# Optimization experiments

Measured on AMD Instinct MI355X. Metric: run time of the kernel, lower is better.

Reference implementation:

```python
import jax, jax.numpy as jnp
import numpy as np

N, E, H, R = 16384, 262144, 256, 64
INV_SQRT_3 = 1.0 / np.sqrt(3.0)
INV_SQRT_H = 1.0 / np.sqrt(float(H))
INV_SQRT_2 = 1.0 / np.sqrt(2.0)


def ssilu(t):
    # ScaledSiLU: silu(x) / 0.6
    return jax.nn.silu(t) * (1.0 / 0.6)


def layernorm(x, g, b):
    m = jnp.mean(x, axis=-1, keepdims=True)
    v = jnp.var(x, axis=-1, keepdims=True)
    return (x - m) * jax.lax.rsqrt(v + 1e-5) * g + b


def gated_equivariant_block(x, v, Wv1, Wv2, Wu1, bu1, Wu2, bu2, out_ch):
    # x: [N, Cin], v: [N, 3, Cin]
    vec1 = jnp.linalg.norm(v @ Wv1, axis=-2)          # [N, Cin]
    vec2 = v @ Wv2                                     # [N, 3, out_ch]
    h = ssilu(jnp.concatenate([x, vec1], axis=-1) @ Wu1 + bu1) @ Wu2 + bu2
    xn, vn = h[..., :out_ch], h[..., out_ch:]
    return ssilu(xn), vn[:, None, :] * vec2


def setup_inputs() -> dict:
    key = jax.random.key(0)
    ks = iter(jax.random.split(key, 48))

    def w(shape, fan_in):
        return jax.random.normal(next(ks), shape, jnp.float32) / np.sqrt(float(fan_in))

    return {
        "x": jax.random.normal(next(ks), (N, H), jnp.float32),
        "vec": jax.random.normal(next(ks), (N, 3, H), jnp.float32),
        "edge_rbf": jax.random.uniform(next(ks), (E, R), jnp.float32),
        "edge_vector": jax.random.normal(next(ks), (E, 3), jnp.float32),
        # PaiNNMessage params
        "ln_g": jnp.ones((H,), jnp.float32), "ln_b": jnp.zeros((H,), jnp.float32),
        "W_x1": w((H, H), H), "b_x1": jnp.zeros((H,), jnp.float32),
        "W_x2": w((H, 3 * H), H), "b_x2": jnp.zeros((3 * H,), jnp.float32),
        "W_rbf": w((R, 3 * H), R), "b_rbf": jnp.zeros((3 * H,), jnp.float32),
        # PaiNNUpdate params
        "W_vp": w((H, 2 * H), H),
        "W_xv1": w((2 * H, H), 2 * H), "b_xv1": jnp.zeros((H,), jnp.float32),
        "W_xv2": w((H, 3 * H), H), "b_xv2": jnp.zeros((3 * H,), jnp.float32),
        # PaiNNOutput block 1 (H -> H//2)
        "o1_Wv1": w((H, H), H), "o1_Wv2": w((H, H // 2), H),
        "o1_Wu1": w((2 * H, H), 2 * H), "o1_bu1": jnp.zeros((H,), jnp.float32),
        "o1_Wu2": w((H, H), H), "o1_bu2": jnp.zeros((H,), jnp.float32),
        # PaiNNOutput block 2 (H//2 -> 1)
        "o2_Wv1": w((H // 2, H // 2), H // 2), "o2_Wv2": w((H // 2, 1), H // 2),
        "o2_Wu1": w((H, H // 2), H), "o2_bu1": jnp.zeros((H // 2,), jnp.float32),
        "o2_Wu2": w((H // 2, 2), H // 2), "o2_bu2": jnp.zeros((2,), jnp.float32),
        "edge_index": jax.random.randint(next(ks), (2, E), 0, N),
    }


def reference(x, vec, edge_rbf, edge_vector,
              ln_g, ln_b, W_x1, b_x1, W_x2, b_x2, W_rbf, b_rbf,
              W_vp, W_xv1, b_xv1, W_xv2, b_xv2,
              o1_Wv1, o1_Wv2, o1_Wu1, o1_bu1, o1_Wu2, o1_bu2,
              o2_Wv1, o2_Wv2, o2_Wu1, o2_bu1, o2_Wu2, o2_bu2,
              edge_index):
    src, dst = edge_index[0], edge_index[1]

    # ---- PaiNNMessage ----
    xh = ssilu(layernorm(x, ln_g, ln_b) @ W_x1 + b_x1) @ W_x2 + b_x2   # [N, 3H]
    rbfh = edge_rbf @ W_rbf + b_rbf                                     # [E, 3H]
    m = xh[src] * rbfh                                                  # gather + fuse
    m1, m2, m3 = m[:, :H], m[:, H:2 * H], m[:, 2 * H:]
    m2 = m2 * INV_SQRT_3
    vmsg = (vec[src] * m2[:, None, :] + m3[:, None, :] * edge_vector[:, :, None]) * INV_SQRT_H  # [E,3,H]
    dx = jax.ops.segment_sum(m1, dst, num_segments=N)
    dvec = jax.ops.segment_sum(vmsg, dst, num_segments=N)
    x = x + dx
    vec = vec + dvec

    # ---- PaiNNUpdate ----
    vp = vec @ W_vp                                    # [N, 3, 2H]
    vec1, vec2 = vp[..., :H], vp[..., H:]
    vec_dot = jnp.sum(vec1 * vec2, axis=1) * INV_SQRT_H            # [N, H]
    vnorm = jnp.sqrt(jnp.sum(vec2 * vec2, axis=-2) + 1e-8)          # [N, H]
    xvh = ssilu(jnp.concatenate([x, vnorm], axis=-1) @ W_xv1 + b_xv1) @ W_xv2 + b_xv2
    xv1, xv2, xv3 = xvh[:, :H], xvh[:, H:2 * H], xvh[:, 2 * H:]
    x = x + (xv1 + xv2 * vec_dot) * INV_SQRT_2
    vec = vec + xv3[:, None, :] * vec1

    # ---- PaiNNOutput ----
    x, vec = gated_equivariant_block(x, vec, o1_Wv1, o1_Wv2, o1_Wu1, o1_bu1, o1_Wu2, o1_bu2, H // 2)
    x, vec = gated_equivariant_block(x, vec, o2_Wv1, o2_Wv2, o2_Wu1, o2_bu1, o2_Wu2, o2_bu2, 1)
    return jnp.squeeze(vec, axis=-1)   # [N, 3]
```

## Files before the change

kernel.cpp:

```cpp
#include <hip/hip_runtime.h>
#include <math.h>

#define NN 16384
#define EE 262144
#define HH 256

#define INV_SQRT_3f 0.57735026918962576f
#define INV_SQRT_Hf 0.0625f
#define INV_SQRT_2f 0.70710678118654752f
#define SSILU_SCALE 1.6666666666666667f

typedef __attribute__((ext_vector_type(8))) short bf16x8;
typedef __attribute__((ext_vector_type(4))) float f32x4;

__device__ __forceinline__ float ssilu_f(float v) {
    return v * (1.0f / (1.0f + __expf(-v))) * SSILU_SCALE;
}
__device__ __forceinline__ float b2f(short s) {
    unsigned int u = ((unsigned int)(unsigned short)s) << 16;
    return __uint_as_float(u);
}
__device__ __forceinline__ short f2b(float f) {
    unsigned int u = __float_as_uint(f);
    unsigned int r = (u + 0x7fff + ((u >> 16) & 1)) >> 16;
    return (short)r;
}
__device__ __forceinline__ void cvt8(float4 a, float4 b, bf16x8& h, bf16x8& l) {
    float v[8] = {a.x, a.y, a.z, a.w, b.x, b.y, b.z, b.w};
    #pragma unroll
    for (int j = 0; j < 8; j++) {
        short hh = f2b(v[j]);
        h[j] = hh;
        l[j] = f2b(v[j] - b2f(hh));
    }
}
__device__ __forceinline__ void cvt8v(f32x4 a, f32x4 b, bf16x8& h, bf16x8& l) {
    float v[8] = {a.x, a.y, a.z, a.w, b.x, b.y, b.z, b.w};
    #pragma unroll
    for (int j = 0; j < 8; j++) {
        short hh = f2b(v[j]);
        h[j] = hh;
        l[j] = f2b(v[j] - b2f(hh));
    }
}

__global__ void __launch_bounds__(256) ln_kernel(const float* __restrict__ x,
                                                 const float* __restrict__ g,
                                                 const float* __restrict__ b,
                                                 float* __restrict__ o_,
                                                 float* __restrict__ x1) {
    int n = blockIdx.x;
    int t = threadIdx.x;
    float v = x[(long)n * HH + t];
    x1[(long)n * HH + t] = v;
    float s = v, s2 = v * v;
    #pragma unroll
    for (int off = 32; off > 0; off >>= 1) {
        s  += __shfl_down(s, off);
        s2 += __shfl_down(s2, off);
    }
    __shared__ float red[8];
    int wave = t >> 6, lane = t & 63;
    if (lane == 0) { red[wave] = s; red[4 + wave] = s2; }
    __syncthreads();
    __shared__ float mr[2];
    if (t == 0) {
        float ts = red[0] + red[1] + red[2] + red[3];
        float ts2 = red[4] + red[5] + red[6] + red[7];
        float mean = ts * (1.0f / HH);
        float var = ts2 * (1.0f / HH) - mean * mean;
        mr[0] = mean;
        mr[1] = rsqrtf(var + 1e-5f);
    }
    __syncthreads();
    o_[(long)n * HH + t] = (v - mr[0]) * mr[1] * g[t] + b[t];
}

struct WtArgs {
    const float* W[12];
    int K[12];
    int N[12];
    int off[13];
};

__global__ void __launch_bounds__(256) wt_split_all(WtArgs a,
                                                    short* __restrict__ WTh,
                                                    short* __restrict__ WTl) {
    int idx = blockIdx.x * 256 + threadIdx.x;
    int s = 0;
    #pragma unroll
    for (int i = 1; i < 12; i++) s += (idx >= a.off[i]) ? 1 : 0;
    int local = idx - a.off[s];
    int K = a.K[s], N = a.N[s];
    int k = local / N, n = local - k * N;
    float w = a.W[s][local];
    short hh = f2b(w);
    long o = (long)a.off[s] + (long)n * K + k;
    WTh[o] = hh;
    WTl[o] = f2b(w - b2f(hh));
}

__global__ void __launch_bounds__(256) mfma_gemm(const float* __restrict__ A,
                                                 const short* __restrict__ Wh,
                                                 const short* __restrict__ Wl,
                                                 const float* __restrict__ bias,
                                                 void* __restrict__ C1,
                                                 void* __restrict__ C2,
                                                 int M, int K, int N, int act) {
    int tid = threadIdx.x;
    int wave = tid >> 6, lane = tid & 63;
    int quad = lane >> 4, l16 = lane & 15;
    long bm = (long)blockIdx.x * 128 + wave * 32;
    long bn = (long)blockIdx.y * 64;
    long a0 = (bm + l16) * K + quad * 8;
    long a1 = a0 + (long)16 * K;
    long w0 = (bn + l16) * K + quad * 8;

    f32x4 acc[2][4];
    #pragma unroll
    for (int f = 0; f < 2; f++)
        #pragma unroll
        for (int t = 0; t < 4; t++) acc[f][t] = (f32x4){0.f, 0.f, 0.f, 0.f};

    bf16x8 cah[2], cal[2], cbh[4], cbl[4];
    cvt8(*(const float4*)(A + a0), *(const float4*)(A + a0 + 4), cah[0], cal[0]);
    cvt8(*(const float4*)(A + a1), *(const float4*)(A + a1 + 4), cah[1], cal[1]);
    #pragma unroll
    for (int t = 0; t < 4; t++) {
        long wo = w0 + (long)t * 16 * K;
        cbh[t] = *(const bf16x8*)(Wh + wo);
        cbl[t] = *(const bf16x8*)(Wl + wo);
    }

    for (int k0 = 0; k0 < K; k0 += 32) {
        int k1 = k0 + 32;
        float4 n0a, n0b, n1a, n1b;
        bf16x8 nbh[4], nbl[4];
        if (k1 < K) {
            n0a = *(const float4*)(A + a0 + k1);
            n0b = *(const float4*)(A + a0 + k1 + 4);
            n1a = *(const float4*)(A + a1 + k1);
            n1b = *(const float4*)(A + a1 + k1 + 4);
            #pragma unroll
            for (int t = 0; t < 4; t++) {
                long wo = w0 + (long)t * 16 * K + k1;
                nbh[t] = *(const bf16x8*)(Wh + wo);
                nbl[t] = *(const bf16x8*)(Wl + wo);
            }
        }
        #pragma unroll
        for (int t = 0; t < 4; t++) {
            #pragma unroll
            for (int f = 0; f < 2; f++) {
                acc[f][t] = __builtin_amdgcn_mfma_f32_16x16x32_bf16(cah[f], cbh[t], acc[f][t], 0, 0, 0);
                acc[f][t] = __builtin_amdgcn_mfma_f32_16x16x32_bf16(cal[f], cbh[t], acc[f][t], 0, 0, 0);
                acc[f][t] = __builtin_amdgcn_mfma_f32_16x16x32_bf16(cah[f], cbl[t], acc[f][t], 0, 0, 0);
            }
        }
        if (k1 < K) {
            cvt8(n0a, n0b, cah[0], cal[0]);
            cvt8(n1a, n1b, cah[1], cal[1]);
            #pragma unroll
            for (int t = 0; t < 4; t++) { cbh[t] = nbh[t]; cbl[t] = nbl[t]; }
        }
    }

    #pragma unroll
    for (int f = 0; f < 2; f++) {
        long row0 = bm + f * 16 + quad * 4;
        #pragma unroll
        for (int t = 0; t < 4; t++) {
            long col = bn + t * 16 + l16;
            float bv = bias ? bias[col] : 0.f;
            #pragma unroll
            for (int r = 0; r < 4; r++) {
                float v = acc[f][t][r] + bv;
                long row = row0 + r;
                if (act == 4) {
                    if (col < 256) ((float*)C1)[row * 256 + col] = v;
                    else           ((short*)C2)[row * 256 + col - 256] = f2b(v);
                } else if (act == 5) {
                    if (col < 256) ((short*)C1)[row * 256 + col] = f2b(v);
                    else           ((float*)C2)[row * 128 + col - 256] = v;
                } else {
                    long idx = row * N + col;
                    if (act == 3) {
                        short hh = f2b(v);
                        ((short*)C1)[idx] = hh;
                        ((short*)C2)[idx] = f2b(v - b2f(hh));
                    } else if (act == 2) {
                        ((short*)C1)[idx] = f2b(v);
                    } else {
                        if (act == 1) v = ssilu_f(v);
                        ((float*)C1)[idx] = v;
                    }
                }
            }
        }
    }
}

__global__ void __launch_bounds__(256) zero_kernel(int* __restrict__ p, int n) {
    int i = blockIdx.x * 256 + threadIdx.x;
    if (i < n) p[i] = 0;
}

__global__ void __launch_bounds__(256) hist_kernel(const int* __restrict__ eidx,
                                                   int* __restrict__ cnt) {
    int e = blockIdx.x * 256 + threadIdx.x;
    atomicAdd(&cnt[eidx[EE + e]], 1);
}

__global__ void __launch_bounds__(256) scan_kernel(int* __restrict__ cursor,
                                                   int* __restrict__ rowptr) {
    int t = threadIdx.x;
    int base_i = t * 64;
    int tsum = 0;
    for (int i = 0; i < 64; i++) tsum += cursor[base_i + i];
    __shared__ int ls[256];
    ls[t] = tsum;
    __syncthreads();
    for (int off = 1; off < 256; off <<= 1) {
        int v = (t >= off) ? ls[t - off] : 0;
        __syncthreads();
        ls[t] += v;
        __syncthreads();
    }
    int running = ls[t] - tsum;
    for (int i = 0; i < 64; i++) {
        int c = cursor[base_i + i];
        rowptr[base_i + i] = running;
        cursor[base_i + i] = running;
        running += c;
    }
    if (t == 255) rowptr[NN] = running;
}

__global__ void __launch_bounds__(256) scatter_kernel(const int* __restrict__ eidx,
                                                      const float* __restrict__ ev,
                                                      int* __restrict__ cursor,
                                                      int* __restrict__ perm,
                                                      int* __restrict__ dsts,
                                                      int* __restrict__ srcs,
                                                      float* __restrict__ evs) {
    int e = blockIdx.x * 256 + threadIdx.x;
    int s_ = eidx[e];
    int d_ = eidx[EE + e];
    int pos = atomicAdd(&cursor[d_], 1);
    perm[pos] = e;
    dsts[pos] = d_;
    srcs[pos] = s_;
    evs[pos * 3 + 0] = ev[e * 3 + 0];
    evs[pos * 3 + 1] = ev[e * 3 + 1];
    evs[pos * 3 + 2] = ev[e * 3 + 2];
}

__global__ void __launch_bounds__(512) edge_gather_kernel(
        const float* __restrict__ rbf,
        const short* __restrict__ Wrh,
        const short* __restrict__ Wrl,
        const float* __restrict__ b_rbf,
        const float* __restrict__ xh,
        const float* __restrict__ vec,
        const int* __restrict__ perm,
        const int* __restrict__ dsts,
        const int* __restrict__ srcs,
        const float* __restrict__ evs,
        float* __restrict__ x1,
        float* __restrict__ vecacc) {
    int tid = threadIdx.x;
    int wave = tid >> 6, lane = tid & 63;
    int quad = lane >> 4, l16 = lane & 15;
    int bm = blockIdx.x * 128;
    int base = wave * 16;

    __shared__ __align__(16) float mlds[128][66];
    __shared__ int dst_s[128], src_s[128];
    __shared__ float ev_s[128][3];

    if (lane < 16) {
        int i = base + lane;
        dst_s[i] = __builtin_nontemporal_load(dsts + bm + i);
        src_s[i] = __builtin_nontemporal_load(srcs + bm + i);
        ev_s[i][0] = __builtin_nontemporal_load(evs + (long)(bm + i) * 3 + 0);
        ev_s[i][1] = __builtin_nontemporal_load(evs + (long)(bm + i) * 3 + 1);
        ev_s[i][2] = __builtin_nontemporal_load(evs + (long)(bm + i) * 3 + 2);
    }

    int e0 = __builtin_nontemporal_load(perm + bm + base + l16);
    bf16x8 afh[2], afl[2];
    {
        long ebase = (long)e0 * 64 + quad * 8;
        #pragma unroll
        for (int ks = 0; ks < 2; ks++) {
            f32x4 ua = __builtin_nontemporal_load(
                reinterpret_cast<const f32x4*>(rbf + ebase + ks * 32));
            f32x4 ub = __builtin_nontemporal_load(
                reinterpret_cast<const f32x4*>(rbf + ebase + ks * 32 + 4));
            cvt8v(ua, ub, afh[ks], afl[ks]);
        }
    }

    for (int sec = 0; sec < 3; sec++) {
        for (int tile = 0; tile < 4; tile++) {
            int bn = sec * 256 + tile * 64;
            f32x4 acc[4];
            #pragma unroll
            for (int t = 0; t < 4; t++) {
                float bv = b_rbf[bn + t * 16 + l16];
                acc[t] = (f32x4){bv, bv, bv, bv};
                #pragma unroll
                for (int ks = 0; ks < 2; ks++) {
                    long wo = (long)(bn + t * 16 + l16) * 64 + ks * 32 + quad * 8;
                    bf16x8 bh = *(const bf16x8*)(Wrh + wo);
                    bf16x8 bl = *(const bf16x8*)(Wrl + wo);
                    acc[t] = __builtin_amdgcn_mfma_f32_16x16x32_bf16(afh[ks], bh, acc[t], 0, 0, 0);
                    acc[t] = __builtin_amdgcn_mfma_f32_16x16x32_bf16(afl[ks], bh, acc[t], 0, 0, 0);
                    acc[t] = __builtin_amdgcn_mfma_f32_16x16x32_bf16(afh[ks], bl, acc[t], 0, 0, 0);
                }
            }
            #pragma unroll
            for (int t = 0; t < 4; t++)
                #pragma unroll
                for (int r = 0; r < 4; r++)
                    mlds[base + quad * 4 + r][t * 16 + l16] = acc[t][r];

            int colx = tile * 64 + lane;
            if (sec == 0) {
                float pv[16];
                #pragma unroll
                for (int i = 0; i < 16; i++) {
                    long xb = (long)src_s[base + i] * 768;
                    pv[i] = mlds[base + i][lane] * xh[xb + colx];
                }
                float a = 0.f;
                int dprev = dst_s[base];
                #pragma unroll
                for (int i = 0; i < 16; i++) {
                    int d = dst_s[base + i];
                    if (d != dprev) {
                        atomicAdd(&x1[(long)dprev * 256 + colx], a);
                        a = 0.f;
                        dprev = d;
                    }
                    a += pv[i];
                }
                atomicAdd(&x1[(long)dprev * 256 + colx], a);
            } else if (sec == 1) {
                float a0 = 0.f, a1 = 0.f, a2 = 0.f;
                int dprev = dst_s[base];
                #pragma unroll 1
                for (int b = 0; b < 4; b++) {
                    float p0[4], p1[4], p2[4];
                    #pragma unroll
                    for (int j = 0; j < 4; j++) {
                        int i = b * 4 + j;
                        long xb = (long)src_s[base + i] * 768;
                        float m2 = mlds[base + i][lane] * (INV_SQRT_3f * INV_SQRT_Hf) *
                                   xh[xb + 256 + colx];
                        p0[j] = vec[xb + colx] * m2;
                        p1[j] = vec[xb + 256 + colx] * m2;
                        p2[j] = vec[xb + 512 + colx] * m2;
                    }
                    #pragma unroll
                    for (int j = 0; j < 4; j++) {
                        int i = b * 4 + j;
                        int d = dst_s[base + i];
                        if (d != dprev) {
                            long vb = (long)dprev * 768 + colx;
                            atomicAdd(&vecacc[vb], a0);
                            atomicAdd(&vecacc[vb + 256], a1);
                            atomicAdd(&vecacc[vb + 512], a2);
                            a0 = a1 = a2 = 0.f;
                            dprev = d;
                        }
                        a0 += p0[j]; a1 += p1[j]; a2 += p2[j];
                    }
                }
                long vb = (long)dprev * 768 + colx;
                atomicAdd(&vecacc[vb], a0);
                atomicAdd(&vecacc[vb + 256], a1);
                atomicAdd(&vecacc[vb + 512], a2);
            } else {
                float pm[16];
                #pragma unroll
                for (int i = 0; i < 16; i++) {
                    long xb = (long)src_s[base + i] * 768;
                    pm[i] = mlds[base + i][lane] * INV_SQRT_Hf * xh[xb + 512 + colx];
                }
                float a0 = 0.f, a1 = 0.f, a2 = 0.f;
                int dprev = dst_s[base];
                #pragma unroll
                for (int i = 0; i < 16; i++) {
                    int d = dst_s[base + i];
                    if (d != dprev) {
                        long vb = (long)dprev * 768 + colx;
                        atomicAdd(&vecacc[vb], a0);
                        atomicAdd(&vecacc[vb + 256], a1);
                        atomicAdd(&vecacc[vb + 512], a2);
                        a0 = a1 = a2 = 0.f;
                        dprev = d;
                    }
                    a0 += pm[i] * ev_s[base + i][0];
                    a1 += pm[i] * ev_s[base + i][1];
                    a2 += pm[i] * ev_s[base + i][2];
                }
                long vb = (long)dprev * 768 + colx;
                atomicAdd(&vecacc[vb], a0);
                atomicAdd(&vecacc[vb + 256], a1);
                atomicAdd(&vecacc[vb + 512], a2);
            }
        }
    }
}

__global__ void __launch_bounds__(256) vdot_cat_kernel(const float* __restrict__ vec1,
                                                       const short* __restrict__ vec2,
                                                       const float* __restrict__ x1,
                                                       float* __restrict__ vdot,
                                                       float* __restrict__ cat) {
    int idx = blockIdx.x * 256 + threadIdx.x;
    int n = idx >> 8, h = idx & 255;
    float dsum = 0.f, s2 = 0.f;
    #pragma unroll
    for (int d = 0; d < 3; d++) {
        long r = (long)(n * 3 + d) * 256 + h;
        float a = vec1[r];
        float b = b2f(vec2[r]);
        dsum += a * b;
        s2 += b * b;
    }
    vdot[idx] = dsum * INV_SQRT_Hf;
    cat[(long)n * 512 + h] = x1[idx];
    cat[(long)n * 512 + 256 + h] = sqrtf(s2 + 1e-8f);
}

__global__ void __launch_bounds__(256) e4_kernel(float* __restrict__ x1,
                                                 float* __restrict__ vecacc,
                                                 const float* __restrict__ vec1,
                                                 const float* __restrict__ vdot,
                                                 const short* __restrict__ xvh_h,
                                                 const short* __restrict__ xvh_l) {
    int idx = blockIdx.x * 256 + threadIdx.x;
    int n = idx >> 8, h = idx & 255;
    long b0 = (long)n * 768 + h;
    float xv1 = b2f(xvh_h[b0])       + b2f(xvh_l[b0]);
    float xv2 = b2f(xvh_h[b0 + 256]) + b2f(xvh_l[b0 + 256]);
    float xv3 = b2f(xvh_h[b0 + 512]) + b2f(xvh_l[b0 + 512]);
    x1[idx] = x1[idx] + (xv1 + xv2 * vdot[idx]) * INV_SQRT_2f;
    #pragma unroll
    for (int d = 0; d < 3; d++) {
        long r = (long)(n * 3 + d) * 256 + h;
        vecacc[r] = vecacc[r] + xv3 * vec1[r];
    }
}

__global__ void __launch_bounds__(256) normcat_kernel(const float* __restrict__ xin,
                                                      const short* __restrict__ w,
                                                      float* __restrict__ cat,
                                                      int Cx, int C, int shift) {
    int idx = blockIdx.x * 256 + threadIdx.x;
    int cols = 1 << shift;
    int n = idx >> shift, c = idx & (cols - 1);
    float v;
    if (c < Cx) {
        v = xin[(long)n * Cx + c];
    } else {
        int cc = c - Cx;
        float s = 0.f;
        #pragma unroll
        for (int d = 0; d < 3; d++) {
            float a = b2f(w[(long)(n * 3 + d) * C + cc]);
            s += a * a;
        }
        v = sqrtf(s);
    }
    cat[idx] = v;
}

__global__ void __launch_bounds__(256) gate1_kernel(const float* __restrict__ h1,
                                                    const float* __restrict__ w2,
                                                    float* __restrict__ x3,
                                                    float* __restrict__ vecC) {
    int idx = blockIdx.x * 256 + threadIdx.x;
    int n = idx >> 7, c = idx & 127;
    x3[idx] = ssilu_f(h1[(long)n * 256 + c]);
    float vn = h1[(long)n * 256 + 128 + c];
    #pragma unroll
    for (int d = 0; d < 3; d++) {
        long r = (long)(n * 3 + d) * 128 + c;
        vecC[r] = vn * w2[r];
    }
}

__global__ void __launch_bounds__(256) g12_kernel(const float* __restrict__ vecC,
                                                  const float* __restrict__ Wv2,
                                                  float* __restrict__ w4) {
    int row = blockIdx.x * 4 + (threadIdx.x >> 6);
    int lane = threadIdx.x & 63;
    long r0 = (long)row * 128 + lane;
    float s = vecC[r0] * Wv2[lane] + vecC[r0 + 64] * Wv2[64 + lane];
    #pragma unroll
    for (int off = 32; off > 0; off >>= 1) s += __shfl_down(s, off);
    if (lane == 0) w4[row] = s;
}

__global__ void __launch_bounds__(256) final_kernel(const float* __restrict__ t5,
                                                    const float* __restrict__ Wu2,
                                                    const float* __restrict__ bu2,
                                                    const float* __restrict__ w4,
                                                    float* __restrict__ out) {
    int n = blockIdx.x * 4 + (threadIdx.x >> 6);
    int lane = threadIdx.x & 63;
    float s = t5[(long)n * 128 + lane] * Wu2[lane * 2 + 1] +
              t5[(long)n * 128 + 64 + lane] * Wu2[(64 + lane) * 2 + 1];
    #pragma unroll
    for (int off = 32; off > 0; off >>= 1) s += __shfl_down(s, off);
    float val = __shfl(s, 0) + bu2[1];
    if (lane < 3) out[(long)n * 3 + lane] = val * w4[(long)n * 3 + lane];
}

extern "C" void kernel_launch(void* const* d_in, const int* in_sizes, int n_in,
                              void* d_out, int out_size, void* d_ws, size_t ws_size,
                              hipStream_t stream) {
    const float* x          = (const float*)d_in[0];
    const float* vec        = (const float*)d_in[1];
    const float* edge_rbf   = (const float*)d_in[2];
    const float* edge_vector= (const float*)d_in[3];
    const float* ln_g       = (const float*)d_in[4];
    const float* ln_b       = (const float*)d_in[5];
    const float* W_x1       = (const float*)d_in[6];
    const float* b_x1       = (const float*)d_in[7];
    const float* W_x2       = (const float*)d_in[8];
    const float* b_x2       = (const float*)d_in[9];
    const float* W_rbf      = (const float*)d_in[10];
    const float* b_rbf      = (const float*)d_in[11];
    const float* W_vp       = (const float*)d_in[12];
    const float* W_xv1      = (const float*)d_in[13];
    const float* b_xv1      = (const float*)d_in[14];
    const float* W_xv2      = (const float*)d_in[15];
    const float* b_xv2      = (const float*)d_in[16];
    const float* o1_Wv1     = (const float*)d_in[17];
    const float* o1_Wv2     = (const float*)d_in[18];
    const float* o1_Wu1     = (const float*)d_in[19];
    const float* o1_bu1     = (const float*)d_in[20];
    const float* o1_Wu2     = (const float*)d_in[21];
    const float* o1_bu2     = (const float*)d_in[22];
    const float* o2_Wv1     = (const float*)d_in[23];
    const float* o2_Wv2     = (const float*)d_in[24];
    const float* o2_Wu1     = (const float*)d_in[25];
    const float* o2_bu1     = (const float*)d_in[26];
    const float* o2_Wu2     = (const float*)d_in[27];
    const float* o2_bu2     = (const float*)d_in[28];
    const int*   edge_index = (const int*)d_in[29];
    float* out = (float*)d_out;
    float* ws  = (float*)d_ws;

    const size_t S = (size_t)NN * 256;
    const size_t Q = S / 4;
    float* x1      = ws;
    float* vecacc  = ws + 4 * Q;
    short* wtb     = (short*)(ws + 16 * Q);
    const long WLO = 1114112;
    float* xln   = ws + 18 * Q;
    float* t1    = ws + 22 * Q;
    float* xh    = ws + 30 * Q;
    int* rowptr    = (int*)(ws + 48 * Q);
    int* cursor    = rowptr + (NN + 1);
    int* perm      = cursor + NN;
    int* dsts      = perm + EE;
    int* srcs      = dsts + EE;
    float* evs     = (float*)(srcs + EE);
    float* vec1  = ws + 30 * Q;
    short* vec2b = (short*)(ws + 42 * Q);
    float* vdot  = ws + 48 * Q;
    float* cat   = ws + 18 * Q;
    float* t2    = ws + 26 * Q;
    short* xvh_h = (short*)(ws + 18 * Q);
    short* xvh_l = (short*)(ws + 42 * Q);
    short* w1b   = (short*)(ws + 30 * Q);
    float* w2    = ws + 36 * Q;
    float* cat2  = ws + 42 * Q;
    float* t4    = ws + 18 * Q;
    float* h1    = ws + 22 * Q;
    float* x3    = ws + 26 * Q;
    float* vecC  = ws + 28 * Q;
    short* w3b   = (short*)(ws + 34 * Q);
    float* w4    = ws + 37 * Q;
    float* cat3  = ws + 38 * Q;
    float* t5    = ws + 42 * Q;

    short* WT_x1    = wtb;
    short* WT_x2    = wtb + 65536;
    short* WT_vp    = wtb + 262144;
    short* WT_xv1   = wtb + 393216;
    short* WT_xv2   = wtb + 524288;
    short* WT_o1Wv1 = wtb + 720896;
    short* WT_o1Wv2 = wtb + 786432;
    short* WT_o1Wu1 = wtb + 819200;
    short* WT_o1Wu2 = wtb + 950272;
    short* WT_o2Wv1 = wtb + 1015808;
    short* WT_o2Wu1 = wtb + 1032192;
    short* WT_rbf   = wtb + 1064960;

    WtArgs wa;
    const float* wsrc[12] = {W_x1, W_x2, W_vp, W_xv1, W_xv2, o1_Wv1, o1_Wv2,
                             o1_Wu1, o1_Wu2, o2_Wv1, o2_Wu1, W_rbf};
    int wk[12] = {256, 256, 256, 512, 256, 256, 256, 512, 256, 128, 256, 64};
    int wn[12] = {256, 768, 512, 256, 768, 256, 128, 256, 256, 128, 128, 768};
    int off = 0;
    for (int i = 0; i < 12; i++) {
        wa.W[i] = wsrc[i]; wa.K[i] = wk[i]; wa.N[i] = wn[i];
        wa.off[i] = off; off += wk[i] * wn[i];
    }
    wa.off[12] = off;
    wt_split_all<<<off / 256, 256, 0, stream>>>(wa, wtb, wtb + WLO);

    hipMemcpyAsync(vecacc, vec, 3 * S * sizeof(float), hipMemcpyDeviceToDevice, stream);

    ln_kernel<<<NN, 256, 0, stream>>>(x, ln_g, ln_b, xln, x1);
    mfma_gemm<<<dim3(NN / 128, 4), 256, 0, stream>>>(xln, WT_x1, WT_x1 + WLO,
                                                     b_x1, t1, nullptr, NN, 256, 256, 1);
    mfma_gemm<<<dim3(NN / 128, 12), 256, 0, stream>>>(t1, WT_x2, WT_x2 + WLO,
                                                      b_x2, xh, nullptr, NN, 256, 768, 0);

    zero_kernel<<<(NN + 255) / 256, 256, 0, stream>>>(cursor, NN);
    hist_kernel<<<EE / 256, 256, 0, stream>>>(edge_index, cursor);
    scan_kernel<<<1, 256, 0, stream>>>(cursor, rowptr);
    scatter_kernel<<<EE / 256, 256, 0, stream>>>(edge_index, edge_vector, cursor,
                                                 perm, dsts, srcs, evs);
    edge_gather_kernel<<<EE / 128, 512, 0, stream>>>(
        edge_rbf, WT_rbf, WT_rbf + WLO, b_rbf, xh, vec,
        perm, dsts, srcs, evs, x1, vecacc);

    mfma_gemm<<<dim3(3 * NN / 128, 8), 256, 0, stream>>>(vecacc, WT_vp, WT_vp + WLO,
                                                         nullptr, vec1, vec2b,
                                                         3 * NN, 256, 512, 4);
    vdot_cat_kernel<<<NN, 256, 0, stream>>>(vec1, vec2b, x1, vdot, cat);
    mfma_gemm<<<dim3(NN / 128, 4), 256, 0, stream>>>(cat, WT_xv1, WT_xv1 + WLO,
                                                     b_xv1, t2, nullptr, NN, 512, 256, 1);
    mfma_gemm<<<dim3(NN / 128, 12), 256, 0, stream>>>(t2, WT_xv2, WT_xv2 + WLO,
                                                      b_xv2, xvh_h, xvh_l, NN, 256, 768, 3);
    e4_kernel<<<NN, 256, 0, stream>>>(x1, vecacc, vec1, vdot, xvh_h, xvh_l);

    mfma_gemm<<<dim3(3 * NN / 128, 6), 256, 0, stream>>>(vecacc, WT_o1Wv1, WT_o1Wv1 + WLO,
                                                         nullptr, w1b, w2,
                                                         3 * NN, 256, 384, 5);
    normcat_kernel<<<NN * 512 / 256, 256, 0, stream>>>(x1, w1b, cat2, 256, 256, 9);
    mfma_gemm<<<dim3(NN / 128, 4), 256, 0, stream>>>(cat2, WT_o1Wu1, WT_o1Wu1 + WLO,
                                                     o1_bu1, t4, nullptr, NN, 512, 256, 1);
    mfma_gemm<<<dim3(NN / 128, 4), 256, 0, stream>>>(t4, WT_o1Wu2, WT_o1Wu2 + WLO,
                                                     o1_bu2, h1, nullptr, NN, 256, 256, 0);
    gate1_kernel<<<NN * 128 / 256, 256, 0, stream>>>(h1, w2, x3, vecC);

    mfma_gemm<<<dim3(3 * NN / 128, 2), 256, 0, stream>>>(vecC, WT_o2Wv1, WT_o2Wv1 + WLO,
                                                         nullptr, w3b, nullptr,
                                                         3 * NN, 128, 128, 2);
    g12_kernel<<<3 * NN / 4, 256, 0, stream>>>(vecC, o2_Wv2, w4);
    normcat_kernel<<<NN * 256 / 256, 256, 0, stream>>>(x3, w3b, cat3, 128, 128, 8);
    mfma_gemm<<<dim3(NN / 128, 2), 256, 0, stream>>>(cat3, WT_o2Wu1, WT_o2Wu1 + WLO,
                                                     o2_bu1, t5, nullptr, NN, 256, 128, 1);
    final_kernel<<<NN / 4, 256, 0, stream>>>(t5, o2_Wu2, o2_bu2, w4, out);
}
```

Before: 1.440 ms.

## Merge vec message sections into one atomic pass and fold vec copy into layernorm

The edge kernel used to handle the m2 (vec gather) and m3 (edge-vector) sections in separate passes, each issuing its own atomicAdds into vecacc. Now both MFMA tiles are computed back to back and their contributions are summed before a single set of atomics, which halves the vec-accumulator atomic traffic and the segmented-reduction work. Separately, the device-to-device memcpy that seeds vecacc with vec is folded into ln_kernel, saving one copy launch. The merged loop keeps the pm2/pm3 arrays live in registers at the same time, which raises register pressure in a 512-thread kernel.

Measured after the change: 1.477 ms. +2.5%, slower.

```diff
diff --git a/kernel.cpp b/kernel.cpp
--- a/kernel.cpp
+++ b/kernel.cpp
@@ -45,14 +45,20 @@
 }
 
 __global__ void __launch_bounds__(256) ln_kernel(const float* __restrict__ x,
+                                                 const float* __restrict__ vec,
                                                  const float* __restrict__ g,
                                                  const float* __restrict__ b,
                                                  float* __restrict__ o_,
-                                                 float* __restrict__ x1) {
+                                                 float* __restrict__ x1,
+                                                 float* __restrict__ vecacc) {
     int n = blockIdx.x;
     int t = threadIdx.x;
     float v = x[(long)n * HH + t];
     x1[(long)n * HH + t] = v;
+    long vb = (long)n * 768 + t;
+    vecacc[vb]       = vec[vb];
+    vecacc[vb + 256] = vec[vb + 256];
+    vecacc[vb + 512] = vec[vb + 512];
     float s = v, s2 = v * v;
     #pragma unroll
     for (int off = 32; off > 0; off >>= 1) {
@@ -255,6 +261,35 @@
     evs[pos * 3 + 2] = ev[e * 3 + 2];
 }
 
+__device__ __forceinline__ void mfma_tile(int bn, int base, int quad, int l16,
+                                          const bf16x8 (&afh)[2],
+                                          const bf16x8 (&afl)[2],
+                                          const short* __restrict__ Wrh,
+                                          const short* __restrict__ Wrl,
+                                          const float* __restrict__ b_rbf,
+                                          float (*mlds)[66]) {
+    f32x4 acc[4];
+    #pragma unroll
+    for (int t = 0; t < 4; t++) {
+        float bv = b_rbf[bn + t * 16 + l16];
+        acc[t] = (f32x4){bv, bv, bv, bv};
+        #pragma unroll
+        for (int ks = 0; ks < 2; ks++) {
+            long wo = (long)(bn + t * 16 + l16) * 64 + ks * 32 + quad * 8;
+            bf16x8 bh = *(const bf16x8*)(Wrh + wo);
+            bf16x8 bl = *(const bf16x8*)(Wrl + wo);
+            acc[t] = __builtin_amdgcn_mfma_f32_16x16x32_bf16(afh[ks], bh, acc[t], 0, 0, 0);
+            acc[t] = __builtin_amdgcn_mfma_f32_16x16x32_bf16(afl[ks], bh, acc[t], 0, 0, 0);
+            acc[t] = __builtin_amdgcn_mfma_f32_16x16x32_bf16(afh[ks], bl, acc[t], 0, 0, 0);
+        }
+    }
+    #pragma unroll
+    for (int t = 0; t < 4; t++)
+        #pragma unroll
+        for (int r = 0; r < 4; r++)
+            mlds[base + quad * 4 + r][t * 16 + l16] = acc[t][r];
+}
+
 __global__ void __launch_bounds__(512) edge_gather_kernel(
         const float* __restrict__ rbf,
         const short* __restrict__ Wrh,
@@ -301,116 +336,79 @@
         }
     }
 
-    for (int sec = 0; sec < 3; sec++) {
-        for (int tile = 0; tile < 4; tile++) {
-            int bn = sec * 256 + tile * 64;
-            f32x4 acc[4];
+    for (int tile = 0; tile < 4; tile++) {
+        mfma_tile(tile * 64, base, quad, l16, afh, afl, Wrh, Wrl, b_rbf, mlds);
+        int colx = tile * 64 + lane;
+        float pv[16];
+        #pragma unroll
+        for (int i = 0; i < 16; i++) {
+            long xb = (long)src_s[base + i] * 768;
+            pv[i] = mlds[base + i][lane] * xh[xb + colx];
+        }
+        float a = 0.f;
+        int dprev = dst_s[base];
+        #pragma unroll
+        for (int i = 0; i < 16; i++) {
+            int d = dst_s[base + i];
+            if (d != dprev) {
+                atomicAdd(&x1[(long)dprev * 256 + colx], a);
+                a = 0.f;
+                dprev = d;
+            }
+            a += pv[i];
+        }
+        atomicAdd(&x1[(long)dprev * 256 + colx], a);
+    }
+
+    for (int tile = 0; tile < 4; tile++) {
+        int colx = tile * 64 + lane;
+        mfma_tile(256 + tile * 64, base, quad, l16, afh, afl, Wrh, Wrl, b_rbf, mlds);
+        float pm2[16];
+        #pragma unroll
+        for (int i = 0; i < 16; i++) {
+            long xb = (long)src_s[base + i] * 768;
+            pm2[i] = mlds[base + i][lane] * (INV_SQRT_3f * INV_SQRT_Hf) *
+                     xh[xb + 256 + colx];
+        }
+        mfma_tile(512 + tile * 64, base, quad, l16, afh, afl, Wrh, Wrl, b_rbf, mlds);
+        float pm3[16];
+        #pragma unroll
+        for (int i = 0; i < 16; i++) {
+            long xb = (long)src_s[base + i] * 768;
+            pm3[i] = mlds[base + i][lane] * INV_SQRT_Hf * xh[xb + 512 + colx];
+        }
+        float a0 = 0.f, a1 = 0.f, a2 = 0.f;
+        int dprev = dst_s[base];
+        #pragma unroll 1
+        for (int b = 0; b < 4; b++) {
+            float p0[4], p1[4], p2[4];
             #pragma unroll
-            for (int t = 0; t < 4; t++) {
-                float bv = b_rbf[bn + t * 16 + l16];
-                acc[t] = (f32x4){bv, bv, bv, bv};
-                #pragma unroll
-                for (int ks = 0; ks < 2; ks++) {
-                    long wo = (long)(bn + t * 16 + l16) * 64 + ks * 32 + quad * 8;
-                    bf16x8 bh = *(const bf16x8*)(Wrh + wo);
-                    bf16x8 bl = *(const bf16x8*)(Wrl + wo);
-                    acc[t] = __builtin_amdgcn_mfma_f32_16x16x32_bf16(afh[ks], bh, acc[t], 0, 0, 0);
-                    acc[t] = __builtin_amdgcn_mfma_f32_16x16x32_bf16(afl[ks], bh, acc[t], 0, 0, 0);
-                    acc[t] = __builtin_amdgcn_mfma_f32_16x16x32_bf16(afh[ks], bl, acc[t], 0, 0, 0);
-                }
+            for (int j = 0; j < 4; j++) {
+                int i = b * 4 + j;
+                long xb = (long)src_s[base + i] * 768;
+                p0[j] = vec[xb + colx] * pm2[i]       + ev_s[base + i][0] * pm3[i];
+                p1[j] = vec[xb + 256 + colx] * pm2[i] + ev_s[base + i][1] * pm3[i];
+                p2[j] = vec[xb + 512 + colx] * pm2[i] + ev_s[base + i][2] * pm3[i];
             }
             #pragma unroll
-            for (int t = 0; t < 4; t++)
-                #pragma unroll
-                for (int r = 0; r < 4; r++)
-                    mlds[base + quad * 4 + r][t * 16 + l16] = acc[t][r];
-
-            int colx = tile * 64 + lane;
-            if (sec == 0) {
-                float pv[16];
-                #pragma unroll
-                for (int i = 0; i < 16; i++) {
-                    long xb = (long)src_s[base + i] * 768;
-                    pv[i] = mlds[base + i][lane] * xh[xb + colx];
+            for (int j = 0; j < 4; j++) {
+                int i = b * 4 + j;
+                int d = dst_s[base + i];
+                if (d != dprev) {
+                    long vb = (long)dprev * 768 + colx;
+                    atomicAdd(&vecacc[vb], a0);
+                    atomicAdd(&vecacc[vb + 256], a1);
+                    atomicAdd(&vecacc[vb + 512], a2);
+                    a0 = a1 = a2 = 0.f;
+                    dprev = d;
                 }
-                float a = 0.f;
-                int dprev = dst_s[base];
-                #pragma unroll
-                for (int i = 0; i < 16; i++) {
-                    int d = dst_s[base + i];
-                    if (d != dprev) {
-                        atomicAdd(&x1[(long)dprev * 256 + colx], a);
-                        a = 0.f;
-                        dprev = d;
-                    }
-                    a += pv[i];
-                }
-                atomicAdd(&x1[(long)dprev * 256 + colx], a);
-            } else if (sec == 1) {
-                float a0 = 0.f, a1 = 0.f, a2 = 0.f;
-                int dprev = dst_s[base];
-                #pragma unroll 1
-                for (int b = 0; b < 4; b++) {
-                    float p0[4], p1[4], p2[4];
-                    #pragma unroll
-                    for (int j = 0; j < 4; j++) {
-                        int i = b * 4 + j;
-                        long xb = (long)src_s[base + i] * 768;
-                        float m2 = mlds[base + i][lane] * (INV_SQRT_3f * INV_SQRT_Hf) *
-                                   xh[xb + 256 + colx];
-                        p0[j] = vec[xb + colx] * m2;
-                        p1[j] = vec[xb + 256 + colx] * m2;
-                        p2[j] = vec[xb + 512 + colx] * m2;
-                    }
-                    #pragma unroll
-                    for (int j = 0; j < 4; j++) {
-                        int i = b * 4 + j;
-                        int d = dst_s[base + i];
-                        if (d != dprev) {
-                            long vb = (long)dprev * 768 + colx;
-                            atomicAdd(&vecacc[vb], a0);
-                            atomicAdd(&vecacc[vb + 256], a1);
-                            atomicAdd(&vecacc[vb + 512], a2);
-                            a0 = a1 = a2 = 0.f;
-                            dprev = d;
-                        }
-                        a0 += p0[j]; a1 += p1[j]; a2 += p2[j];
-                    }
-                }
-                long vb = (long)dprev * 768 + colx;
-                atomicAdd(&vecacc[vb], a0);
-                atomicAdd(&vecacc[vb + 256], a1);
-                atomicAdd(&vecacc[vb + 512], a2);
-            } else {
-                float pm[16];
-                #pragma unroll
-                for (int i = 0; i < 16; i++) {
-                    long xb = (long)src_s[base + i] * 768;
-                    pm[i] = mlds[base + i][lane] * INV_SQRT_Hf * xh[xb + 512 + colx];
-                }
-                float a0 = 0.f, a1 = 0.f, a2 = 0.f;
-                int dprev = dst_s[base];
-                #pragma unroll
-                for (int i = 0; i < 16; i++) {
-                    int d = dst_s[base + i];
-                    if (d != dprev) {
-                        long vb = (long)dprev * 768 + colx;
-                        atomicAdd(&vecacc[vb], a0);
-                        atomicAdd(&vecacc[vb + 256], a1);
-                        atomicAdd(&vecacc[vb + 512], a2);
-                        a0 = a1 = a2 = 0.f;
-                        dprev = d;
-                    }
-                    a0 += pm[i] * ev_s[base + i][0];
-                    a1 += pm[i] * ev_s[base + i][1];
-                    a2 += pm[i] * ev_s[base + i][2];
-                }
-                long vb = (long)dprev * 768 + colx;
-                atomicAdd(&vecacc[vb], a0);
-                atomicAdd(&vecacc[vb + 256], a1);
-                atomicAdd(&vecacc[vb + 512], a2);
+                a0 += p0[j]; a1 += p1[j]; a2 += p2[j];
             }
         }
+        long vb = (long)dprev * 768 + colx;
+        atomicAdd(&vecacc[vb], a0);
+        atomicAdd(&vecacc[vb + 256], a1);
+        atomicAdd(&vecacc[vb + 512], a2);
     }
 }
 
@@ -616,9 +614,7 @@
     wa.off[12] = off;
     wt_split_all<<<off / 256, 256, 0, stream>>>(wa, wtb, wtb + WLO);
 
-    hipMemcpyAsync(vecacc, vec, 3 * S * sizeof(float), hipMemcpyDeviceToDevice, stream);
-
-    ln_kernel<<<NN, 256, 0, stream>>>(x, ln_g, ln_b, xln, x1);
+    ln_kernel<<<NN, 256, 0, stream>>>(x, vec, ln_g, ln_b, xln, x1, vecacc);
     mfma_gemm<<<dim3(NN / 128, 4), 256, 0, stream>>>(xln, WT_x1, WT_x1 + WLO,
                                                      b_x1, t1, nullptr, NN, 256, 256, 1);
     mfma_gemm<<<dim3(NN / 128, 12), 256, 0, stream>>>(t1, WT_x2, WT_x2 + WLO,
```
